# Performance work log

Hardware: AMD Instinct MI355X
Metric: run time of the kernel (lower is better)

Reference implementation:

```python
import jax, jax.numpy as jnp
import numpy as np

B, T, I, H = 128, 1024, 256, 512


def setup_inputs() -> dict:
    key = jax.random.key(0)
    ks = jax.random.split(key, 4)
    x = jax.random.normal(ks[0], (B, T, I), dtype=jnp.float32)
    h = jax.random.normal(ks[1], (1, B, H), dtype=jnp.float32)
    # torch Linear default init ~ U(-1/sqrt(fan_in), 1/sqrt(fan_in)); use small randn
    W_ih = jax.random.normal(ks[2], (3 * H, I), dtype=jnp.float32) * (1.0 / np.sqrt(I))
    W_hh = jax.random.normal(ks[3], (3 * H, H), dtype=jnp.float32) * (1.0 / np.sqrt(H))
    b_ih = jnp.zeros((3 * H,), dtype=jnp.float32)
    b_hh = jnp.zeros((3 * H,), dtype=jnp.float32)
    return {"x": x, "h": h, "W_ih": W_ih, "b_ih": b_ih, "W_hh": W_hh, "b_hh": b_hh}


def _gru_scan(x, h0, W_ih, b_ih, W_hh, b_hh):
    Bq, Tq, _ = x.shape
    Hq = W_hh.shape[1]
    # precompute input projections for all timesteps (same math, one big GEMM)
    x_proj = jnp.einsum('bti,gi->tbg', x, W_ih)  # (T, B, 3H)
    r_bi, z_bi, n_bi = jnp.split(b_ih, 3)
    r_bh, z_bh, n_bh = jnp.split(b_hh, 3)

    def step(carry, xp):
        # carry is the 4H cat [r, z, n, h]; only last H (hidden) feeds recurrence
        h = carry[:, -Hq:]
        hp = h @ W_hh.T  # (B, 3H)
        r_i, z_i, n_i = jnp.split(xp, 3, axis=1)
        r_h, z_h, n_h = jnp.split(hp, 3, axis=1)
        r = jax.nn.sigmoid(r_i + r_bi + r_h + r_bh)
        z = jax.nn.sigmoid(z_i + z_bi + z_h + z_bh)
        n = jnp.tanh(n_i + n_bi + r * (n_h + n_bh))
        new_h = (1.0 - z) * n + z * h
        new_carry = jnp.concatenate([r, z, n, new_h], axis=1)
        return new_carry, None

    init = jnp.concatenate([jnp.zeros((Bq, 3 * Hq), x.dtype), h0], axis=1)
    final, _ = jax.lax.scan(step, init, x_proj)
    return final  # (B, 4H)


def reference(x, h, W_ih, b_ih, W_hh, b_hh):
    Bq = x.shape[0]
    final = _gru_scan(x, h[0], W_ih, b_ih, W_hh, b_hh)
    return (final.reshape(Bq, 1, -1), final.reshape(1, Bq, -1))
```

## Files before the change

### kernel.cpp

```cpp
#include <hip/hip_runtime.h>

typedef float v2f __attribute__((ext_vector_type(2)));

#define B_Q 128
#define T_Q 1024
#define I_Q 256
#define H_Q 512

#define NGR    8
#define BG     16
#define JW     8
#define NWG    512
#define NTHR   256
#define WPG    (NWG / NGR)
#define C1     (B_Q * 4 * H_Q)

#define CH_STR  10
#define ROW_STR 640
#define HT_FLOATS (BG * ROW_STR)
#define TB_FLOATS (BG * 9)
#define LDS_FLOATS (HT_FLOATS + TB_FLOATS)
#define LDS_BYTES  (LDS_FLOATS * 4)

template<int M>
__device__ __forceinline__ float partner(float t) {
    if constexpr (M == 16)
        return __int_as_float(__builtin_amdgcn_ds_swizzle(__float_as_int(t), 0x401F));
    else if constexpr (M == 8)
        return __int_as_float(__builtin_amdgcn_update_dpp(0, __float_as_int(t), 0x128, 0xF, 0xF, true));
    else if constexpr (M == 4)
        return __int_as_float(__builtin_amdgcn_ds_swizzle(__float_as_int(t), 0x101F));
    else if constexpr (M == 2)
        return __int_as_float(__builtin_amdgcn_update_dpp(0, __float_as_int(t), 0x4E, 0xF, 0xF, true));
    else
        return __int_as_float(__builtin_amdgcn_update_dpp(0, __float_as_int(t), 0xB1, 0xF, 0xF, true));
}

template<int M, int N>
__device__ __forceinline__ void bstage(float* v, bool hi) {
    #pragma unroll
    for (int i = 0; i < N / 2; ++i) {
        float keep = hi ? v[i + N / 2] : v[i];
        float send = hi ? v[i]         : v[i + N / 2];
        v[i] = keep + partner<M>(send);
    }
}
__device__ __forceinline__ void bflychunk(float* v, int kg) {
    #pragma unroll
    for (int i = 0; i < 16; ++i) v[i] += partner<16>(v[i]);
    bstage<8, 16>(v, (kg & 8) != 0);
    bstage<4, 8 >(v, (kg & 4) != 0);
    bstage<2, 4 >(v, (kg & 2) != 0);
    bstage<1, 2 >(v, (kg & 1) != 0);
}

__device__ __forceinline__ void bfly16(float* v) {
    #pragma unroll
    for (int i = 0; i < 8; ++i) v[i] += partner<8>(v[i + 8]);
    #pragma unroll
    for (int i = 0; i < 4; ++i) v[i] += partner<4>(v[i + 4]);
    v[0] += partner<2>(v[2]);
    v[1] += partner<2>(v[3]);
    v[0] += partner<1>(v[1]);
    v[0] += partner<16>(v[0]);
}

__device__ __forceinline__ float fsig(float x) {
    return __builtin_amdgcn_rcpf(1.f + __builtin_amdgcn_exp2f(-1.44269504088896f * x));
}
__device__ __forceinline__ float ftanh(float x) {
    return 1.f - 2.f * __builtin_amdgcn_rcpf(1.f + __builtin_amdgcn_exp2f(2.88539008177793f * x));
}

extern "C" __global__ void __launch_bounds__(NTHR, 2)
__attribute__((amdgpu_num_vgpr(128)))
gru_scan_kernel(const float* __restrict__ x,
                const float* __restrict__ h0,
                const float* __restrict__ Wih,
                const float* __restrict__ bih,
                const float* __restrict__ Whh,
                const float* __restrict__ bhh,
                float* __restrict__ out,
                int* __restrict__ flags)
{
    extern __shared__ float lds[];
    float* Ht   = lds;
    float* tbuf = lds + HT_FLOATS;

    const int wg  = blockIdx.x;
    const int g   = wg >> 6;
    const int s   = wg & 63;
    const int tid = threadIdx.x;
    const int j   = tid >> 5;
    const int kg  = tid & 31;
    const int jg  = s * JW + j;
    const int c15 = kg & 15;

    float* hbuf = out + C1 + (size_t)g * (BG * 4 * H_Q);
    int*   gflags = flags + g * WPG;

    v2f wh[3][8];
    v2f wi[3][4];
    #pragma unroll
    for (int gt = 0; gt < 3; ++gt) {
        const float* wr = Whh + (size_t)(gt * H_Q + jg) * H_Q + 8 * kg;
        float4 t0 = *(const float4*)(wr);
        float4 t1 = *(const float4*)(wr + 4);
        float4 t2 = *(const float4*)(wr + 256);
        float4 t3 = *(const float4*)(wr + 260);
        wh[gt][0] = (v2f){t0.x, t0.y}; wh[gt][1] = (v2f){t0.z, t0.w};
        wh[gt][2] = (v2f){t1.x, t1.y}; wh[gt][3] = (v2f){t1.z, t1.w};
        wh[gt][4] = (v2f){t2.x, t2.y}; wh[gt][5] = (v2f){t2.z, t2.w};
        wh[gt][6] = (v2f){t3.x, t3.y}; wh[gt][7] = (v2f){t3.z, t3.w};
        const float* wx = Wih + (size_t)(gt * H_Q + jg) * I_Q + 8 * kg;
        float4 u0 = *(const float4*)(wx);
        float4 u1 = *(const float4*)(wx + 4);
        wi[gt][0] = (v2f){u0.x, u0.y}; wi[gt][1] = (v2f){u0.z, u0.w};
        wi[gt][2] = (v2f){u1.x, u1.y}; wi[gt][3] = (v2f){u1.z, u1.w};
    }

    const float br = bih[jg]           + bhh[jg];
    const float bz = bih[H_Q + jg]     + bhh[H_Q + jg];
    const float bin = bih[2 * H_Q + jg], bhn = bhh[2 * H_Q + jg];

    const size_t xstr_b = (size_t)T_Q * I_Q;
    const float* xbase  = x + (size_t)(g * BG) * xstr_b + 8 * kg;

    float lr = 0.f, lz = 0.f, ln = 0.f, lh = 0.f;

    for (int t = 1; t <= T_Q; ++t) {
        float pr[BG], pz[BG], pn[BG];
        const float* xt = xbase + (size_t)(t - 1) * I_Q;
        #pragma unroll
        for (int i = 0; i < BG; ++i) {
            const float* xp = xt + (size_t)i * xstr_b;
            float4 xa4 = *(const float4*)(xp);
            float4 xb4 = *(const float4*)(xp + 4);
            v2f x0 = (v2f){xa4.x, xa4.y}, x1 = (v2f){xa4.z, xa4.w};
            v2f x2 = (v2f){xb4.x, xb4.y}, x3 = (v2f){xb4.z, xb4.w};
            v2f sr = x0 * wi[0][0] + x1 * wi[0][1] + x2 * wi[0][2] + x3 * wi[0][3];
            v2f sz = x0 * wi[1][0] + x1 * wi[1][1] + x2 * wi[1][2] + x3 * wi[1][3];
            v2f sn = x0 * wi[2][0] + x1 * wi[2][1] + x2 * wi[2][2] + x3 * wi[2][3];
            pr[i] = sr.x + sr.y;
            pz[i] = sz.x + sz.y;
            pn[i] = sn.x + sn.y;
        }
        bflychunk(pr, kg); bflychunk(pz, kg); bflychunk(pn, kg);
        const float oxr = pr[0], oxz = pz[0], oxn = pn[0];

        if (t == 1) {
            const unsigned long long* src =
                (const unsigned long long*)(h0 + (size_t)(g * BG) * H_Q);
            #pragma unroll
            for (int i = 0; i < BG; ++i) {
                int q = tid + i * NTHR;
                int b = q >> 8, qr = q & 255;
                unsigned long long v = src[q];
                *(unsigned long long*)(Ht + b * ROW_STR + (qr >> 2) * CH_STR
                                       + ((qr & 3) << 1)) = v;
            }
        } else {
            if (tid < WPG) {
                int cnt = 0;
                while (__hip_atomic_load(gflags + tid, __ATOMIC_RELAXED,
                                         __HIP_MEMORY_SCOPE_AGENT) < t - 1) {
                    __builtin_amdgcn_s_sleep(1);
                    if (++cnt > 100000000) break;
                }
            }
            __syncthreads();
            const unsigned long long* src = (const unsigned long long*)
                (hbuf + (size_t)((t - 1) & 1) * (BG * H_Q));
            #pragma unroll
            for (int i = 0; i < BG; ++i) {
                int q = tid + i * NTHR;
                int b = q >> 8, qr = q & 255;
                unsigned long long v = __hip_atomic_load(src + q, __ATOMIC_RELAXED,
                                                         __HIP_MEMORY_SCOPE_AGENT);
                *(unsigned long long*)(Ht + b * ROW_STR + (qr >> 2) * CH_STR
                                       + ((qr & 3) << 1)) = v;
            }
        }
        __syncthreads();

        #pragma unroll
        for (int i = 0; i < BG; ++i) {
            const float* hp = Ht + (i ^ c15) * ROW_STR + CH_STR * kg;
            v2f a0 = *(const v2f*)(hp);
            v2f a1 = *(const v2f*)(hp + 2);
            v2f a2 = *(const v2f*)(hp + 4);
            v2f a3 = *(const v2f*)(hp + 6);
            const float* hq = hp + 32 * CH_STR;
            v2f c0 = *(const v2f*)(hq);
            v2f c1 = *(const v2f*)(hq + 2);
            v2f c2 = *(const v2f*)(hq + 4);
            v2f c3 = *(const v2f*)(hq + 6);
            v2f sr = a0 * wh[0][0] + a1 * wh[0][1] + a2 * wh[0][2] + a3 * wh[0][3]
                   + c0 * wh[0][4] + c1 * wh[0][5] + c2 * wh[0][6] + c3 * wh[0][7];
            v2f sz = a0 * wh[1][0] + a1 * wh[1][1] + a2 * wh[1][2] + a3 * wh[1][3]
                   + c0 * wh[1][4] + c1 * wh[1][5] + c2 * wh[1][6] + c3 * wh[1][7];
            v2f sn = a0 * wh[2][0] + a1 * wh[2][1] + a2 * wh[2][2] + a3 * wh[2][3]
                   + c0 * wh[2][4] + c1 * wh[2][5] + c2 * wh[2][6] + c3 * wh[2][7];
            pr[i] = sr.x + sr.y;
            pz[i] = sz.x + sz.y;
            pn[i] = sn.x + sn.y;
        }
        bfly16(pr); bfly16(pz); bfly16(pn);

        float hx = Ht[c15 * ROW_STR + (jg >> 3) * CH_STR + (jg & 7)];

        float rg = fsig(oxr + pr[0] + br);
        float zg = fsig(oxz + pz[0] + bz);
        float ng = ftanh(oxn + bin + rg * (pn[0] + bhn));
        float hn = (1.f - zg) * ng + zg * hx;

        if (kg < 16) tbuf[kg * 9 + j] = hn;
        __syncthreads();
        if (tid < 64) {
            float* dst = hbuf + (size_t)(t & 1) * (BG * H_Q);
            #pragma unroll
            for (int u = 0; u < 2; ++u) {
                int q = tid + u * 64;
                int b = q >> 3, jl = q & 7;
                __hip_atomic_store(dst + b * H_Q + s * JW + jl, tbuf[b * 9 + jl],
                                   __ATOMIC_RELAXED, __HIP_MEMORY_SCOPE_AGENT);
            }
            asm volatile("s_waitcnt vmcnt(0)" ::: "memory");
            if (tid == 0)
                __hip_atomic_store(gflags + s, t, __ATOMIC_RELAXED,
                                   __HIP_MEMORY_SCOPE_AGENT);
        }

        lr = rg; lz = zg; ln = ng; lh = hn;
    }

    if (tid < WPG) {
        int cnt = 0;
        while (__hip_atomic_load(gflags + tid, __ATOMIC_RELAXED,
                                 __HIP_MEMORY_SCOPE_AGENT) < T_Q) {
            __builtin_amdgcn_s_sleep(2);
            if (++cnt > 100000000) break;
        }
    }
    __syncthreads();

    if (kg < 16) {
        size_t o = (size_t)(g * BG + kg) * (4 * H_Q);
        out[o + jg]             = lr;
        out[o + H_Q + jg]       = lz;
        out[o + 2 * H_Q + jg]   = ln;
        out[o + 3 * H_Q + jg]   = lh;
        size_t o2 = o + (size_t)C1;
        out[o2 + jg]            = lr;
        out[o2 + H_Q + jg]      = lz;
        out[o2 + 2 * H_Q + jg]  = ln;
        out[o2 + 3 * H_Q + jg]  = lh;
    }
}

extern "C" void kernel_launch(void* const* d_in, const int* in_sizes, int n_in,
                              void* d_out, int out_size, void* d_ws, size_t ws_size,
                              hipStream_t stream) {
    const float* x   = (const float*)d_in[0];
    const float* h0  = (const float*)d_in[1];
    const float* Wih = (const float*)d_in[2];
    const float* bih = (const float*)d_in[3];
    const float* Whh = (const float*)d_in[4];
    const float* bhh = (const float*)d_in[5];
    float* outp  = (float*)d_out;
    int*   flags = (int*)d_ws;

    (void)in_sizes; (void)n_in; (void)ws_size; (void)out_size;

    hipMemsetAsync(d_ws, 0, NWG * sizeof(int), stream);

    gru_scan_kernel<<<dim3(NWG), dim3(NTHR), LDS_BYTES, stream>>>(
        x, h0, Wih, bih, Whh, bhh, outp, flags);
}
```

Before: 9.419 ms.

## Pad LDS hidden rows to odd stride and map groups onto XCD pairs

Changes the LDS chunk stride from 10 to 9 floats so that per-lane reads of the hidden state hit different banks, using 4-byte-aligned v2f accesses in place of 8-byte-aligned ones. It also remaps workgroup IDs so that each batch group's 64 workgroups sit on a pair of XCDs instead of being spread round-robin across all of them. The aim is to cut LDS bank conflicts and to make the cross-workgroup flag and hidden-state exchange stay more local to a shared L2. The odd stride may split ds_read_b64 into two ds_read_b32 instructions, which could raise the LDS instruction count.

```diff
diff --git a/kernel.cpp b/kernel.cpp
--- a/kernel.cpp
+++ b/kernel.cpp
@@ -1,6 +1,7 @@
 #include <hip/hip_runtime.h>
 
 typedef float v2f __attribute__((ext_vector_type(2)));
+typedef v2f v2f_u __attribute__((aligned(4)));
 
 #define B_Q 128
 #define T_Q 1024
@@ -15,8 +16,8 @@
 #define WPG    (NWG / NGR)
 #define C1     (B_Q * 4 * H_Q)
 
-#define CH_STR  10
-#define ROW_STR 640
+#define CH_STR  9
+#define ROW_STR 576
 #define HT_FLOATS (BG * ROW_STR)
 #define TB_FLOATS (BG * 9)
 #define LDS_FLOATS (HT_FLOATS + TB_FLOATS)
@@ -88,8 +89,11 @@
     float* tbuf = lds + HT_FLOATS;
 
     const int wg  = blockIdx.x;
-    const int g   = wg >> 6;
-    const int s   = wg & 63;
+    const int xcd = wg & 7;
+    const int r   = wg >> 3;
+    const int p   = xcd >> 1;
+    const int g   = 2 * p + ((xcd & 1) ^ (r >> 5));
+    const int s   = r;
     const int tid = threadIdx.x;
     const int j   = tid >> 5;
     const int kg  = tid & 31;
@@ -155,9 +159,10 @@
             for (int i = 0; i < BG; ++i) {
                 int q = tid + i * NTHR;
                 int b = q >> 8, qr = q & 255;
-                unsigned long long v = src[q];
-                *(unsigned long long*)(Ht + b * ROW_STR + (qr >> 2) * CH_STR
-                                       + ((qr & 3) << 1)) = v;
+                union { unsigned long long u; float f[2]; } cv;
+                cv.u = src[q];
+                *(v2f_u*)(Ht + b * ROW_STR + (qr >> 2) * CH_STR
+                          + ((qr & 3) << 1)) = (v2f_u){cv.f[0], cv.f[1]};
             }
         } else {
             if (tid < WPG) {
@@ -175,10 +180,11 @@
             for (int i = 0; i < BG; ++i) {
                 int q = tid + i * NTHR;
                 int b = q >> 8, qr = q & 255;
-                unsigned long long v = __hip_atomic_load(src + q, __ATOMIC_RELAXED,
-                                                         __HIP_MEMORY_SCOPE_AGENT);
-                *(unsigned long long*)(Ht + b * ROW_STR + (qr >> 2) * CH_STR
-                                       + ((qr & 3) << 1)) = v;
+                union { unsigned long long u; float f[2]; } cv;
+                cv.u = __hip_atomic_load(src + q, __ATOMIC_RELAXED,
+                                         __HIP_MEMORY_SCOPE_AGENT);
+                *(v2f_u*)(Ht + b * ROW_STR + (qr >> 2) * CH_STR
+                          + ((qr & 3) << 1)) = (v2f_u){cv.f[0], cv.f[1]};
             }
         }
         __syncthreads();
@@ -186,15 +192,15 @@
         #pragma unroll
         for (int i = 0; i < BG; ++i) {
             const float* hp = Ht + (i ^ c15) * ROW_STR + CH_STR * kg;
-            v2f a0 = *(const v2f*)(hp);
-            v2f a1 = *(const v2f*)(hp + 2);
-            v2f a2 = *(const v2f*)(hp + 4);
-            v2f a3 = *(const v2f*)(hp + 6);
+            v2f a0 = *(const v2f_u*)(hp);
+            v2f a1 = *(const v2f_u*)(hp + 2);
+            v2f a2 = *(const v2f_u*)(hp + 4);
+            v2f a3 = *(const v2f_u*)(hp + 6);
             const float* hq = hp + 32 * CH_STR;
-            v2f c0 = *(const v2f*)(hq);
-            v2f c1 = *(const v2f*)(hq + 2);
-            v2f c2 = *(const v2f*)(hq + 4);
-            v2f c3 = *(const v2f*)(hq + 6);
+            v2f c0 = *(const v2f_u*)(hq);
+            v2f c1 = *(const v2f_u*)(hq + 2);
+            v2f c2 = *(const v2f_u*)(hq + 4);
+            v2f c3 = *(const v2f_u*)(hq + 6);
             v2f sr = a0 * wh[0][0] + a1 * wh[0][1] + a2 * wh[0][2] + a3 * wh[0][3]
                    + c0 * wh[0][4] + c1 * wh[0][5] + c2 * wh[0][6] + c3 * wh[0][7];
             v2f sz = a0 * wh[1][0] + a1 * wh[1][1] + a2 * wh[1][2] + a3 * wh[1][3]
```

After: 9.473 ms. About the same (+0.6%).

## Split each workgroup across two batch groups with XCD-aware mapping and interleaved phases

Applied to the files above, without the earlier changes.

Each workgroup now processes two half-groups of 8 batch rows (from two different 16-row groups) in alternating phases within each timestep, instead of one 16-row group. Workgroups are mapped by blockIdx modulo 8 so that all workgroups exchanging hidden state through global memory and flags sit on the same XCD, keeping spin-wait traffic local. The B-phase load and compute run while other workgroups finish the A-phase, which is meant to hide the barrier latency of each half. In exchange there are more __syncthreads per step, the flag wait only covers both halves jointly, and the cross-XCD placement depends on the round-robin dispatch assumption.

```diff
diff --git a/kernel.cpp b/kernel.cpp
--- a/kernel.cpp
+++ b/kernel.cpp
@@ -1,25 +1,23 @@
 #include <hip/hip_runtime.h>
 
 typedef float v2f __attribute__((ext_vector_type(2)));
+typedef unsigned long long ull;
 
 #define B_Q 128
 #define T_Q 1024
 #define I_Q 256
 #define H_Q 512
 
-#define NGR    8
-#define BG     16
+#define BH     8
 #define JW     8
 #define NWG    512
 #define NTHR   256
-#define WPG    (NWG / NGR)
 #define C1     (B_Q * 4 * H_Q)
 
 #define CH_STR  10
 #define ROW_STR 640
-#define HT_FLOATS (BG * ROW_STR)
-#define TB_FLOATS (BG * 9)
-#define LDS_FLOATS (HT_FLOATS + TB_FLOATS)
+#define HT_FLOATS (16 * ROW_STR)
+#define LDS_FLOATS (HT_FLOATS + 2 * 72)
 #define LDS_BYTES  (LDS_FLOATS * 4)
 
 template<int M>
@@ -45,23 +43,23 @@
         v[i] = keep + partner<M>(send);
     }
 }
-__device__ __forceinline__ void bflychunk(float* v, int kg) {
-    #pragma unroll
-    for (int i = 0; i < 16; ++i) v[i] += partner<16>(v[i]);
-    bstage<8, 16>(v, (kg & 8) != 0);
-    bstage<4, 8 >(v, (kg & 4) != 0);
-    bstage<2, 4 >(v, (kg & 2) != 0);
-    bstage<1, 2 >(v, (kg & 1) != 0);
-}
-
-__device__ __forceinline__ void bfly16(float* v) {
-    #pragma unroll
-    for (int i = 0; i < 8; ++i) v[i] += partner<8>(v[i + 8]);
+__device__ __forceinline__ void bflychunk8(float* v, int kg) {
+    #pragma unroll
+    for (int i = 0; i < 8; ++i) v[i] += partner<16>(v[i]);
+    #pragma unroll
+    for (int i = 0; i < 8; ++i) v[i] += partner<8>(v[i]);
+    bstage<4, 8>(v, (kg & 4) != 0);
+    bstage<2, 4>(v, (kg & 2) != 0);
+    bstage<1, 2>(v, (kg & 1) != 0);
+}
+
+__device__ __forceinline__ void bfly8x(float* v) {
     #pragma unroll
     for (int i = 0; i < 4; ++i) v[i] += partner<4>(v[i + 4]);
     v[0] += partner<2>(v[2]);
     v[1] += partner<2>(v[3]);
     v[0] += partner<1>(v[1]);
+    v[0] += partner<8>(v[0]);
     v[0] += partner<16>(v[0]);
 }
 
@@ -70,6 +68,63 @@
 }
 __device__ __forceinline__ float ftanh(float x) {
     return 1.f - 2.f * __builtin_amdgcn_rcpf(1.f + __builtin_amdgcn_exp2f(2.88539008177793f * x));
+}
+
+__device__ __forceinline__ void xpart(const float* xt, size_t xstr_b,
+                                      const v2f (*wi)[4], int kg, float* ox) {
+    float pr[BH], pz[BH], pn[BH];
+    #pragma unroll
+    for (int i = 0; i < BH; ++i) {
+        const float* xp = xt + (size_t)i * xstr_b;
+        float4 xa4 = *(const float4*)(xp);
+        float4 xb4 = *(const float4*)(xp + 4);
+        v2f x0 = (v2f){xa4.x, xa4.y}, x1 = (v2f){xa4.z, xa4.w};
+        v2f x2 = (v2f){xb4.x, xb4.y}, x3 = (v2f){xb4.z, xb4.w};
+        v2f sr = x0 * wi[0][0] + x1 * wi[0][1] + x2 * wi[0][2] + x3 * wi[0][3];
+        v2f sz = x0 * wi[1][0] + x1 * wi[1][1] + x2 * wi[1][2] + x3 * wi[1][3];
+        v2f sn = x0 * wi[2][0] + x1 * wi[2][1] + x2 * wi[2][2] + x3 * wi[2][3];
+        pr[i] = sr.x + sr.y; pz[i] = sz.x + sz.y; pn[i] = sn.x + sn.y;
+    }
+    bflychunk8(pr, kg); bflychunk8(pz, kg); bflychunk8(pn, kg);
+    ox[0] = pr[0]; ox[1] = pz[0]; ox[2] = pn[0];
+}
+
+__device__ __forceinline__ void hpart(const float* Hrow0, const v2f (*wh)[8],
+                                      int kg, int c7, float* oh) {
+    float pr[BH], pz[BH], pn[BH];
+    #pragma unroll
+    for (int i = 0; i < BH; ++i) {
+        const float* hp = Hrow0 + (i ^ c7) * ROW_STR + CH_STR * kg;
+        v2f a0 = *(const v2f*)(hp);
+        v2f a1 = *(const v2f*)(hp + 2);
+        v2f a2 = *(const v2f*)(hp + 4);
+        v2f a3 = *(const v2f*)(hp + 6);
+        const float* hq = hp + 32 * CH_STR;
+        v2f c0 = *(const v2f*)(hq);
+        v2f c1 = *(const v2f*)(hq + 2);
+        v2f c2 = *(const v2f*)(hq + 4);
+        v2f c3 = *(const v2f*)(hq + 6);
+        v2f sr = a0 * wh[0][0] + a1 * wh[0][1] + a2 * wh[0][2] + a3 * wh[0][3]
+               + c0 * wh[0][4] + c1 * wh[0][5] + c2 * wh[0][6] + c3 * wh[0][7];
+        v2f sz = a0 * wh[1][0] + a1 * wh[1][1] + a2 * wh[1][2] + a3 * wh[1][3]
+               + c0 * wh[1][4] + c1 * wh[1][5] + c2 * wh[1][6] + c3 * wh[1][7];
+        v2f sn = a0 * wh[2][0] + a1 * wh[2][1] + a2 * wh[2][2] + a3 * wh[2][3]
+               + c0 * wh[2][4] + c1 * wh[2][5] + c2 * wh[2][6] + c3 * wh[2][7];
+        pr[i] = sr.x + sr.y; pz[i] = sz.x + sz.y; pn[i] = sn.x + sn.y;
+    }
+    bfly8x(pr); bfly8x(pz); bfly8x(pn);
+    oh[0] = pr[0]; oh[1] = pz[0]; oh[2] = pn[0];
+}
+
+__device__ __forceinline__ void stageHalf(const ull* src, float* HtRows, int tid) {
+    #pragma unroll
+    for (int i = 0; i < BH; ++i) {
+        int q = tid + i * NTHR;
+        int b = q >> 8, qr = q & 255;
+        ull v = __hip_atomic_load(src + q, __ATOMIC_RELAXED,
+                                  __HIP_MEMORY_SCOPE_AGENT);
+        *(ull*)(HtRows + b * ROW_STR + (qr >> 2) * CH_STR + ((qr & 3) << 1)) = v;
+    }
 }
 
 extern "C" __global__ void __launch_bounds__(NTHR, 2)
@@ -84,20 +139,26 @@
                 int* __restrict__ flags)
 {
     extern __shared__ float lds[];
-    float* Ht   = lds;
-    float* tbuf = lds + HT_FLOATS;
+    float* Ht    = lds;
+    float* tbufA = lds + HT_FLOATS;
+    float* tbufB = tbufA + 72;
 
     const int wg  = blockIdx.x;
-    const int g   = wg >> 6;
-    const int s   = wg & 63;
+    const int xcd = wg & 7;
+    const int r   = wg >> 3;
+    const int p   = xcd >> 1;
+    const int hf  = xcd & 1;
+    const int s   = r;
+    const int gA  = 2 * p, gB = 2 * p + 1;
     const int tid = threadIdx.x;
     const int j   = tid >> 5;
     const int kg  = tid & 31;
     const int jg  = s * JW + j;
-    const int c15 = kg & 15;
-
-    float* hbuf = out + C1 + (size_t)g * (BG * 4 * H_Q);
-    int*   gflags = flags + g * WPG;
+    const int c7  = kg & 7;
+
+    float* hbufA = out + C1 + (size_t)gA * (16 * 4 * H_Q);
+    float* hbufB = out + C1 + (size_t)gB * (16 * 4 * H_Q);
+    int*   pflags = flags + (p * 2 + hf) * 64;
 
     v2f wh[3][8];
     v2f wi[3][4];
@@ -124,119 +185,95 @@
     const float bin = bih[2 * H_Q + jg], bhn = bhh[2 * H_Q + jg];
 
     const size_t xstr_b = (size_t)T_Q * I_Q;
-    const float* xbase  = x + (size_t)(g * BG) * xstr_b + 8 * kg;
-
-    float lr = 0.f, lz = 0.f, ln = 0.f, lh = 0.f;
+    const float* xbaseA = x + (size_t)(gA * 16 + hf * BH) * xstr_b + 8 * kg;
+    const float* xbaseB = x + (size_t)(gB * 16 + hf * BH) * xstr_b + 8 * kg;
+
+    float lrA = 0, lzA = 0, lnA = 0, lhA = 0;
+    float lrB = 0, lzB = 0, lnB = 0, lhB = 0;
 
     for (int t = 1; t <= T_Q; ++t) {
-        float pr[BG], pz[BG], pn[BG];
-        const float* xt = xbase + (size_t)(t - 1) * I_Q;
-        #pragma unroll
-        for (int i = 0; i < BG; ++i) {
-            const float* xp = xt + (size_t)i * xstr_b;
-            float4 xa4 = *(const float4*)(xp);
-            float4 xb4 = *(const float4*)(xp + 4);
-            v2f x0 = (v2f){xa4.x, xa4.y}, x1 = (v2f){xa4.z, xa4.w};
-            v2f x2 = (v2f){xb4.x, xb4.y}, x3 = (v2f){xb4.z, xb4.w};
-            v2f sr = x0 * wi[0][0] + x1 * wi[0][1] + x2 * wi[0][2] + x3 * wi[0][3];
-            v2f sz = x0 * wi[1][0] + x1 * wi[1][1] + x2 * wi[1][2] + x3 * wi[1][3];
-            v2f sn = x0 * wi[2][0] + x1 * wi[2][1] + x2 * wi[2][2] + x3 * wi[2][3];
-            pr[i] = sr.x + sr.y;
-            pz[i] = sz.x + sz.y;
-            pn[i] = sn.x + sn.y;
-        }
-        bflychunk(pr, kg); bflychunk(pz, kg); bflychunk(pn, kg);
-        const float oxr = pr[0], oxz = pz[0], oxn = pn[0];
+        float oxA[3];
+        xpart(xbaseA + (size_t)(t - 1) * I_Q, xstr_b, wi, kg, oxA);
 
         if (t == 1) {
-            const unsigned long long* src =
-                (const unsigned long long*)(h0 + (size_t)(g * BG) * H_Q);
-            #pragma unroll
-            for (int i = 0; i < BG; ++i) {
-                int q = tid + i * NTHR;
-                int b = q >> 8, qr = q & 255;
-                unsigned long long v = src[q];
-                *(unsigned long long*)(Ht + b * ROW_STR + (qr >> 2) * CH_STR
-                                       + ((qr & 3) << 1)) = v;
-            }
+            stageHalf((const ull*)(h0 + (size_t)(gA * 16 + hf * BH) * H_Q), Ht, tid);
         } else {
-            if (tid < WPG) {
+            if (tid < 64) {
                 int cnt = 0;
-                while (__hip_atomic_load(gflags + tid, __ATOMIC_RELAXED,
+                while (__hip_atomic_load(pflags + tid, __ATOMIC_RELAXED,
                                          __HIP_MEMORY_SCOPE_AGENT) < t - 1) {
                     __builtin_amdgcn_s_sleep(1);
                     if (++cnt > 100000000) break;
                 }
             }
             __syncthreads();
-            const unsigned long long* src = (const unsigned long long*)
-                (hbuf + (size_t)((t - 1) & 1) * (BG * H_Q));
-            #pragma unroll
-            for (int i = 0; i < BG; ++i) {
-                int q = tid + i * NTHR;
-                int b = q >> 8, qr = q & 255;
-                unsigned long long v = __hip_atomic_load(src + q, __ATOMIC_RELAXED,
-                                                         __HIP_MEMORY_SCOPE_AGENT);
-                *(unsigned long long*)(Ht + b * ROW_STR + (qr >> 2) * CH_STR
-                                       + ((qr & 3) << 1)) = v;
-            }
+            stageHalf((const ull*)(hbufA + (size_t)((t - 1) & 1) * (16 * H_Q)
+                                   + (size_t)hf * BH * H_Q), Ht, tid);
         }
         __syncthreads();
 
-        #pragma unroll
-        for (int i = 0; i < BG; ++i) {
-            const float* hp = Ht + (i ^ c15) * ROW_STR + CH_STR * kg;
-            v2f a0 = *(const v2f*)(hp);
-            v2f a1 = *(const v2f*)(hp + 2);
-            v2f a2 = *(const v2f*)(hp + 4);
-            v2f a3 = *(const v2f*)(hp + 6);
-            const float* hq = hp + 32 * CH_STR;
-            v2f c0 = *(const v2f*)(hq);
-            v2f c1 = *(const v2f*)(hq + 2);
-            v2f c2 = *(const v2f*)(hq + 4);
-            v2f c3 = *(const v2f*)(hq + 6);
-            v2f sr = a0 * wh[0][0] + a1 * wh[0][1] + a2 * wh[0][2] + a3 * wh[0][3]
-                   + c0 * wh[0][4] + c1 * wh[0][5] + c2 * wh[0][6] + c3 * wh[0][7];
-            v2f sz = a0 * wh[1][0] + a1 * wh[1][1] + a2 * wh[1][2] + a3 * wh[1][3]
-                   + c0 * wh[1][4] + c1 * wh[1][5] + c2 * wh[1][6] + c3 * wh[1][7];
-            v2f sn = a0 * wh[2][0] + a1 * wh[2][1] + a2 * wh[2][2] + a3 * wh[2][3]
-                   + c0 * wh[2][4] + c1 * wh[2][5] + c2 * wh[2][6] + c3 * wh[2][7];
-            pr[i] = sr.x + sr.y;
-            pz[i] = sz.x + sz.y;
-            pn[i] = sn.x + sn.y;
-        }
-        bfly16(pr); bfly16(pz); bfly16(pn);
-
-        float hx = Ht[c15 * ROW_STR + (jg >> 3) * CH_STR + (jg & 7)];
-
-        float rg = fsig(oxr + pr[0] + br);
-        float zg = fsig(oxz + pz[0] + bz);
-        float ng = ftanh(oxn + bin + rg * (pn[0] + bhn));
-        float hn = (1.f - zg) * ng + zg * hx;
-
-        if (kg < 16) tbuf[kg * 9 + j] = hn;
+        float ohA[3];
+        hpart(Ht, wh, kg, c7, ohA);
+        float hxA = Ht[c7 * ROW_STR + (jg >> 3) * CH_STR + (jg & 7)];
+        float rgA = fsig(oxA[0] + ohA[0] + br);
+        float zgA = fsig(oxA[1] + ohA[1] + bz);
+        float ngA = ftanh(oxA[2] + bin + rgA * (ohA[2] + bhn));
+        float hnA = (1.f - zgA) * ngA + zgA * hxA;
+
+        if (kg < 8) tbufA[kg * 9 + j] = hnA;
         __syncthreads();
         if (tid < 64) {
-            float* dst = hbuf + (size_t)(t & 1) * (BG * H_Q);
-            #pragma unroll
-            for (int u = 0; u < 2; ++u) {
-                int q = tid + u * 64;
-                int b = q >> 3, jl = q & 7;
-                __hip_atomic_store(dst + b * H_Q + s * JW + jl, tbuf[b * 9 + jl],
-                                   __ATOMIC_RELAXED, __HIP_MEMORY_SCOPE_AGENT);
-            }
+            float* dst = hbufA + (size_t)(t & 1) * (16 * H_Q)
+                       + (size_t)hf * BH * H_Q;
+            int b = tid >> 3, jl = tid & 7;
+            __hip_atomic_store(dst + b * H_Q + s * JW + jl, tbufA[b * 9 + jl],
+                               __ATOMIC_RELAXED, __HIP_MEMORY_SCOPE_AGENT);
+        }
+
+        float oxB[3];
+        xpart(xbaseB + (size_t)(t - 1) * I_Q, xstr_b, wi, kg, oxB);
+
+        if (t == 1) {
+            stageHalf((const ull*)(h0 + (size_t)(gB * 16 + hf * BH) * H_Q),
+                      Ht + 8 * ROW_STR, tid);
+        } else {
+            stageHalf((const ull*)(hbufB + (size_t)((t - 1) & 1) * (16 * H_Q)
+                                   + (size_t)hf * BH * H_Q),
+                      Ht + 8 * ROW_STR, tid);
+        }
+        __syncthreads();
+
+        float ohB[3];
+        hpart(Ht + 8 * ROW_STR, wh, kg, c7, ohB);
+        float hxB = Ht[(8 + c7) * ROW_STR + (jg >> 3) * CH_STR + (jg & 7)];
+        float rgB = fsig(oxB[0] + ohB[0] + br);
+        float zgB = fsig(oxB[1] + ohB[1] + bz);
+        float ngB = ftanh(oxB[2] + bin + rgB * (ohB[2] + bhn));
+        float hnB = (1.f - zgB) * ngB + zgB * hxB;
+
+        if (kg < 8) tbufB[kg * 9 + j] = hnB;
+        __syncthreads();
+        if (tid < 64) {
+            float* dst = hbufB + (size_t)(t & 1) * (16 * H_Q)
+                       + (size_t)hf * BH * H_Q;
+            int b = tid >> 3, jl = tid & 7;
+            __hip_atomic_store(dst + b * H_Q + s * JW + jl, tbufB[b * 9 + jl],
+                               __ATOMIC_RELAXED, __HIP_MEMORY_SCOPE_AGENT);
             asm volatile("s_waitcnt vmcnt(0)" ::: "memory");
             if (tid == 0)
-                __hip_atomic_store(gflags + s, t, __ATOMIC_RELAXED,
+                __hip_atomic_store(pflags + s, t, __ATOMIC_RELAXED,
                                    __HIP_MEMORY_SCOPE_AGENT);
         }
 
-        lr = rg; lz = zg; ln = ng; lh = hn;
-    }
-
-    if (tid < WPG) {
+        if (t == T_Q) {
+            lrA = rgA; lzA = zgA; lnA = ngA; lhA = hnA;
+            lrB = rgB; lzB = zgB; lnB = ngB; lhB = hnB;
+        }
+    }
+
+    if (tid < 128) {
         int cnt = 0;
-        while (__hip_atomic_load(gflags + tid, __ATOMIC_RELAXED,
+        while (__hip_atomic_load(flags + p * 128 + tid, __ATOMIC_RELAXED,
                                  __HIP_MEMORY_SCOPE_AGENT) < T_Q) {
             __builtin_amdgcn_s_sleep(2);
             if (++cnt > 100000000) break;
@@ -244,17 +281,25 @@
     }
     __syncthreads();
 
-    if (kg < 16) {
-        size_t o = (size_t)(g * BG + kg) * (4 * H_Q);
-        out[o + jg]             = lr;
-        out[o + H_Q + jg]       = lz;
-        out[o + 2 * H_Q + jg]   = ln;
-        out[o + 3 * H_Q + jg]   = lh;
-        size_t o2 = o + (size_t)C1;
-        out[o2 + jg]            = lr;
-        out[o2 + H_Q + jg]      = lz;
-        out[o2 + 2 * H_Q + jg]  = ln;
-        out[o2 + 3 * H_Q + jg]  = lh;
+    if (kg < 8) {
+        size_t oA = (size_t)(gA * 16 + hf * BH + kg) * (4 * H_Q);
+        out[oA + jg]            = lrA;
+        out[oA + H_Q + jg]      = lzA;
+        out[oA + 2 * H_Q + jg]  = lnA;
+        out[oA + 3 * H_Q + jg]  = lhA;
+        out[oA + C1 + jg]           = lrA;
+        out[oA + C1 + H_Q + jg]     = lzA;
+        out[oA + C1 + 2 * H_Q + jg] = lnA;
+        out[oA + C1 + 3 * H_Q + jg] = lhA;
+        size_t oB = (size_t)(gB * 16 + hf * BH + kg) * (4 * H_Q);
+        out[oB + jg]            = lrB;
+        out[oB + H_Q + jg]      = lzB;
+        out[oB + 2 * H_Q + jg]  = lnB;
+        out[oB + 3 * H_Q + jg]  = lhB;
+        out[oB + C1 + jg]           = lrB;
+        out[oB + C1 + H_Q + jg]     = lzB;
+        out[oB + C1 + 2 * H_Q + jg] = lnB;
+        out[oB + C1 + 3 * H_Q + jg] = lhB;
     }
 }
 
```

Result: slower. 10.02 ms (+6.4%).
